# Optimization experiments

Hardware: AMD Instinct MI355X
Metric: run time of the kernel (lower is better)

## Reference

```python
import jax, jax.numpy as jnp
import numpy as np

D, E, H, K = 1024, 8, 1024, 2          # d_model, num_experts, hidden_size, top_k
NUM_LAYERS, LB_W, Z_W = 16, 0.01, 0.001
B, S = 2, 2048


def setup_inputs() -> dict:
    key = jax.random.key(0)
    ks = jax.random.split(key, 8)
    s = lambda d: 1.0 / np.sqrt(d)
    return {
        "x": jax.random.normal(ks[0], (B, S, D), jnp.float32),
        "w_router": jax.random.normal(ks[1], (D, E), jnp.float32) * s(D),
        "w1": jax.random.normal(ks[2], (E, D, H), jnp.float32) * s(D),
        "w3": jax.random.normal(ks[3], (E, D, H), jnp.float32) * s(D),
        "w2": jax.random.normal(ks[4], (E, H, D), jnp.float32) * s(H),
        "sw1": jax.random.normal(ks[5], (D, H), jnp.float32) * s(D),
        "sw3": jax.random.normal(ks[6], (D, H), jnp.float32) * s(D),
        "sw2": jax.random.normal(ks[7], (H, D), jnp.float32) * s(H),
    }


def reference(x, w_router, w1, w3, w2, sw1, sw3, sw2):
    b, s_len, _ = x.shape
    xt = x.reshape(-1, D)                       # (N, D) flattened tokens
    n_tok = xt.shape[0]

    # ---- router: softmax over experts, then top-k ----
    logits = xt @ w_router                      # (N, E)
    probs = jax.nn.softmax(logits, axis=-1)
    weights, indices = jax.lax.top_k(probs, K)  # (N, K)

    # combine weights scattered back to dense (N, E) form
    onehot = jax.nn.one_hot(indices, E, dtype=x.dtype)    # (N, K, E)
    cw = jnp.einsum("nk,nke->ne", weights, onehot)       # (N, E)
    counts = jnp.sum(onehot, axis=(0, 1))                 # (E,) tokens per expert

    # ---- expert SwiGLU MLPs (dense dispatch, weighted combine) ----
    g = jnp.einsum("nd,edh->neh", xt, w1)                 # (N, E, H)
    u = jnp.einsum("nd,edh->neh", xt, w3)
    h = jax.nn.silu(g) * u
    eout = jnp.einsum("neh,ehd->ned", h, w2)              # (N, E, D)
    out = jnp.einsum("ne,ned->nd", cw, eout)              # (N, D)

    # ---- shared expert, weighted-sum combine with top_k ----
    shared = (jax.nn.silu(xt @ sw1) * (xt @ sw3)) @ sw2   # (N, D)
    out = (out * K + shared) / (K + 1)

    # ---- aux losses (training mode) ----
    logits32 = logits.astype(jnp.float32)
    scale = E * LB_W / (NUM_LAYERS * n_tok * K)
    lb_loss = scale * jnp.dot(counts.astype(jnp.float32),
                              jax.nn.softmax(logits32, axis=-1).sum(axis=0))
    z_loss = jnp.mean(jnp.square(jax.nn.logsumexp(logits32, axis=-1))) * Z_W

    return out.reshape(b, s_len, D), lb_loss, z_loss
```

## Files before the change

kernel.cpp:

```cpp
#include <hip/hip_runtime.h>

#define NTOK 4096
#define NEXP 8
#define MAXTILES 104

typedef __attribute__((ext_vector_type(8))) short short8;
typedef __attribute__((ext_vector_type(4))) float f32x4;
typedef __attribute__((ext_vector_type(4))) unsigned int uint4v;
typedef __attribute__((ext_vector_type(2))) unsigned int uint2v;

__device__ __forceinline__ unsigned short f2bf(float f) {
  union { float f; unsigned u; } v; v.f = f;
  unsigned u = v.u;
  return (unsigned short)((u + 0x7FFFu + ((u >> 16) & 1u)) >> 16);
}

__device__ __forceinline__ void gll16(const void* g, void* l) {
  __builtin_amdgcn_global_load_lds((const __attribute__((address_space(1))) void*)g,
                                   (__attribute__((address_space(3))) void*)l, 16, 0, 0);
}

__global__ __launch_bounds__(256) void prep_k(
    const float* __restrict__ w1, const float* __restrict__ w3, const float* __restrict__ w2,
    const float* __restrict__ sw1, const float* __restrict__ sw3, const float* __restrict__ sw2,
    unsigned short* __restrict__ dst,
    const float* __restrict__ x, const float* __restrict__ wr, unsigned short* __restrict__ xb,
    int* __restrict__ rec, float* __restrict__ wts, float* __restrict__ probs,
    float* __restrict__ lsebuf) {
  __shared__ unsigned short tile[64][65];
  int b = blockIdx.x;
  if (b < 6912) {
    int z = b >> 8, rem = b & 255;
    int r0 = (rem >> 4) * 64, c0 = (rem & 15) * 64;
    const float* S;
    if (z < 8) S = w1 + (size_t)z * 1048576;
    else if (z < 16) S = w3 + (size_t)(z - 8) * 1048576;
    else if (z < 24) S = w2 + (size_t)(z - 16) * 1048576;
    else S = (z == 24) ? sw1 : (z == 25) ? sw3 : sw2;
    unsigned short* Dp = dst + (size_t)z * 1048576;
    int t = threadIdx.x;
    int r = t >> 2, cb = (t & 3) * 16;
    const float* sp = S + (size_t)(r0 + r) * 1024 + c0 + cb;
    f32x4 v0 = ((const f32x4*)sp)[0], v1 = ((const f32x4*)sp)[1];
    f32x4 v2 = ((const f32x4*)sp)[2], v3 = ((const f32x4*)sp)[3];
#pragma unroll
    for (int j = 0; j < 4; ++j) {
      tile[r][cb + j] = f2bf(v0[j]);
      tile[r][cb + 4 + j] = f2bf(v1[j]);
      tile[r][cb + 8 + j] = f2bf(v2[j]);
      tile[r][cb + 12 + j] = f2bf(v3[j]);
    }
    __syncthreads();
    unsigned short* dp = Dp + (size_t)(c0 + r) * 1024 + r0 + cb;
    uint4v o0, o1;
#pragma unroll
    for (int j = 0; j < 4; ++j) {
      o0[j] = (unsigned)tile[cb + 2 * j][r] | ((unsigned)tile[cb + 2 * j + 1][r] << 16);
      o1[j] = (unsigned)tile[cb + 8 + 2 * j][r] | ((unsigned)tile[cb + 9 + 2 * j][r] << 16);
    }
    ((uint4v*)dp)[0] = o0;
    ((uint4v*)dp)[1] = o1;
  } else {
    int t = threadIdx.x, lane = t & 63, wv = t >> 6;
    int tok = (b - 6912) * 4 + wv;
    const f32x4* x4 = (const f32x4*)(x + (size_t)tok * 1024);
    f32x4 xv[4];
#pragma unroll
    for (int j = 0; j < 4; ++j) xv[j] = x4[j * 64 + lane];

    unsigned short* xo = xb + (size_t)tok * 1024;
#pragma unroll
    for (int j = 0; j < 4; ++j) {
      uint2v o;
      o[0] = (unsigned)f2bf(xv[j][0]) | ((unsigned)f2bf(xv[j][1]) << 16);
      o[1] = (unsigned)f2bf(xv[j][2]) | ((unsigned)f2bf(xv[j][3]) << 16);
      *(uint2v*)(xo + j * 256 + lane * 4) = o;
    }

    float acc[NEXP];
#pragma unroll
    for (int e = 0; e < NEXP; ++e) acc[e] = 0.f;
#pragma unroll
    for (int j = 0; j < 4; ++j) {
      int base = j * 256 + lane * 4;
#pragma unroll
      for (int c = 0; c < 4; ++c) {
        float xf = xv[j][c];
        const f32x4* wp = (const f32x4*)(wr + (size_t)(base + c) * NEXP);
        f32x4 q0 = wp[0], q1 = wp[1];
#pragma unroll
        for (int e = 0; e < 4; ++e) { acc[e] += xf * q0[e]; acc[4 + e] += xf * q1[e]; }
      }
    }
#pragma unroll
    for (int off = 32; off > 0; off >>= 1) {
#pragma unroll
      for (int e = 0; e < NEXP; ++e) acc[e] += __shfl_xor(acc[e], off);
    }

    float mx = acc[0];
#pragma unroll
    for (int e = 1; e < NEXP; ++e) mx = fmaxf(mx, acc[e]);
    float s = 0.f;
#pragma unroll
    for (int e = 0; e < NEXP; ++e) s += __expf(acc[e] - mx);
    float inv = 1.f / s;

    if (lane < NEXP) probs[(size_t)tok * NEXP + lane] = __expf(acc[lane] - mx) * inv;
    if (lane == 0) {
      int i0 = 0; float v0 = acc[0];
#pragma unroll
      for (int e = 1; e < NEXP; ++e) if (acc[e] > v0) { v0 = acc[e]; i0 = e; }
      int i1 = -1; float v1 = -3.4e38f;
#pragma unroll
      for (int e = 0; e < NEXP; ++e) if (e != i0 && acc[e] > v1) { v1 = acc[e]; i1 = e; }
      rec[tok] = i0 | (i1 << 8);
      wts[2 * tok] = __expf(v0 - mx) * inv;
      wts[2 * tok + 1] = __expf(v1 - mx) * inv;
      lsebuf[tok] = mx + __logf(s);
    }
  }
}

__global__ __launch_bounds__(1024) void build_k(
    const int* __restrict__ rec, const float* __restrict__ wts, const float* __restrict__ probs,
    const float* __restrict__ lsebuf,
    int* __restrict__ tlist, float* __restrict__ wlist,
    int* __restrict__ counts, int* __restrict__ ebase, int* __restrict__ tiles,
    float* __restrict__ lossout) {
  __shared__ int lcnt[NEXP];
  __shared__ float sprob[NEXP];
  __shared__ float sz;
  int t = threadIdx.x, lane = t & 63;
  if (t < NEXP) { lcnt[t] = 0; sprob[t] = 0.f; }
  if (t == 0) sz = 0.f;
  __syncthreads();

  float pacc[NEXP];
#pragma unroll
  for (int e = 0; e < NEXP; ++e) pacc[e] = 0.f;
  float zacc = 0.f;

#pragma unroll
  for (int it = 0; it < 4; ++it) {
    int tok = t + it * 1024;
    int r = rec[tok];
    int i0 = r & 255, i1 = (r >> 8) & 255;
    int p0 = atomicAdd(&lcnt[i0], 1);
    tlist[i0 * NTOK + p0] = tok;
    wlist[i0 * NTOK + p0] = wts[2 * tok];
    int p1 = atomicAdd(&lcnt[i1], 1);
    tlist[i1 * NTOK + p1] = tok | (1 << 16);
    wlist[i1 * NTOK + p1] = wts[2 * tok + 1];
    f32x4 a = ((const f32x4*)(probs + (size_t)tok * NEXP))[0];
    f32x4 c = ((const f32x4*)(probs + (size_t)tok * NEXP))[1];
#pragma unroll
    for (int j = 0; j < 4; ++j) { pacc[j] += a[j]; pacc[4 + j] += c[j]; }
    float lv = lsebuf[tok];
    zacc += lv * lv;
  }
#pragma unroll
  for (int off = 32; off > 0; off >>= 1) {
#pragma unroll
    for (int e = 0; e < NEXP; ++e) pacc[e] += __shfl_xor(pacc[e], off);
    zacc += __shfl_xor(zacc, off);
  }
  if (lane == 0) {
#pragma unroll
    for (int e = 0; e < NEXP; ++e) atomicAdd(&sprob[e], pacc[e]);
    atomicAdd(&sz, zacc);
  }
  __syncthreads();

  if (t == 0) {
    int a = 0, tt = 0;
    float dot = 0.f;
    for (int e = 0; e < NEXP; ++e) {
      counts[e] = lcnt[e];
      ebase[e] = a;
      int nt = (lcnt[e] + 127) >> 7;
      for (int i = 0; i < nt; ++i) tiles[tt++] = (e << 16) | i;
      a += nt * 128;
      dot += (float)lcnt[e] * sprob[e];
    }
    ebase[NEXP] = a;
    for (int i = 0; i < 32; ++i) tiles[tt++] = (NEXP << 16) | i;
    while (tt < MAXTILES) tiles[tt++] = -1;
    lossout[0] = 6.103515625e-7f * dot;
    lossout[1] = sz * (0.001f / 4096.f);
  }
}

__global__ __launch_bounds__(256, 3) void gemm1_k(
    const unsigned short* __restrict__ xb,
    const unsigned short* __restrict__ w1T, const unsigned short* __restrict__ w3T,
    const unsigned short* __restrict__ sw1T, const unsigned short* __restrict__ sw3T,
    unsigned short* __restrict__ hout,
    const int* __restrict__ tlist, const int* __restrict__ counts,
    const int* __restrict__ ebase, const int* __restrict__ tiles) {
  int td = tiles[blockIdx.y];
  if (td < 0) return;
  const int e = td >> 16;
  const int m0 = (td & 0xFFFF) << 7;
  const int n0 = blockIdx.x * 64;
  const bool sh = (e == NEXP);
  const int n_e = sh ? NTOK : counts[e];
  const int hb = ebase[e];
  const unsigned short* B1p = sh ? sw1T : w1T + (size_t)e * 1048576;
  const unsigned short* B3p = sh ? sw3T : w3T + (size_t)e * 1048576;
  const int* listp = tlist + e * NTOK;

  __shared__ unsigned short As[128 * 64], Bs1[64 * 64], Bs3[64 * 64];
  const int tid = threadIdx.x, lane = tid & 63, wv = tid >> 6;
  const int wrw = wv >> 1, wc = wv & 1, l16 = lane & 15, lq = lane >> 4;

  const unsigned short* ga[4];
#pragma unroll
  for (int i = 0; i < 4; ++i) {
    int c = tid + i * 256;
    int r = c >> 3, ks = (c & 7) ^ (r & 7);
    int ar = m0 + r;
    int rowA = sh ? ar : (ar < n_e ? (listp[ar] & 0xFFFF) : 0);
    ga[i] = xb + (size_t)rowA * 1024 + ks * 8;
  }
  const unsigned short* gb[2];
  const unsigned short* gc[2];
#pragma unroll
  for (int i = 0; i < 2; ++i) {
    int c = tid + i * 256;
    int r = c >> 3, ks = (c & 7) ^ (r & 7);
    gb[i] = B1p + (size_t)(n0 + r) * 1024 + ks * 8;
    gc[i] = B3p + (size_t)(n0 + r) * 1024 + ks * 8;
  }
  unsigned short* lA[4];
#pragma unroll
  for (int i = 0; i < 4; ++i) lA[i] = As + i * 2048 + wv * 512;
  unsigned short* lB[2] = {Bs1 + wv * 512, Bs1 + 2048 + wv * 512};
  unsigned short* lC[2] = {Bs3 + wv * 512, Bs3 + 2048 + wv * 512};

  f32x4 accg[4][2], accu[4][2];
#pragma unroll
  for (int mi = 0; mi < 4; ++mi)
#pragma unroll
    for (int ni = 0; ni < 2; ++ni)
#pragma unroll
      for (int r = 0; r < 4; ++r) { accg[mi][ni][r] = 0.f; accu[mi][ni][r] = 0.f; }

  for (int k0 = 0; k0 < 1024; k0 += 64) {
#pragma unroll
    for (int i = 0; i < 4; ++i) { gll16(ga[i], lA[i]); ga[i] += 64; }
#pragma unroll
    for (int i = 0; i < 2; ++i) { gll16(gb[i], lB[i]); gb[i] += 64; gll16(gc[i], lC[i]); gc[i] += 64; }
    __syncthreads();
#pragma unroll
    for (int kh = 0; kh < 2; ++kh) {
      short8 af[4], b1f[2], b3f[2];
#pragma unroll
      for (int mi = 0; mi < 4; ++mi) {
        int R = wrw * 64 + mi * 16 + l16;
        int s = (kh * 4 + lq) ^ (R & 7);
        af[mi] = *(const short8*)&As[R * 64 + s * 8];
      }
#pragma unroll
      for (int ni = 0; ni < 2; ++ni) {
        int R = wc * 32 + ni * 16 + l16;
        int s = (kh * 4 + lq) ^ (R & 7);
        b1f[ni] = *(const short8*)&Bs1[R * 64 + s * 8];
        b3f[ni] = *(const short8*)&Bs3[R * 64 + s * 8];
      }
#pragma unroll
      for (int mi = 0; mi < 4; ++mi)
#pragma unroll
        for (int ni = 0; ni < 2; ++ni) {
          accg[mi][ni] = __builtin_amdgcn_mfma_f32_16x16x32_bf16(af[mi], b1f[ni], accg[mi][ni], 0, 0, 0);
          accu[mi][ni] = __builtin_amdgcn_mfma_f32_16x16x32_bf16(af[mi], b3f[ni], accu[mi][ni], 0, 0, 0);
        }
    }
    __syncthreads();
  }

#pragma unroll
  for (int mi = 0; mi < 4; ++mi)
#pragma unroll
    for (int ni = 0; ni < 2; ++ni) {
      int col = n0 + wc * 32 + ni * 16 + l16;
#pragma unroll
      for (int r = 0; r < 4; ++r) {
        int row = m0 + wrw * 64 + mi * 16 + lq * 4 + r;
        float g = accg[mi][ni][r], u = accu[mi][ni][r];
        float h = g / (1.f + __expf(-g)) * u;
        hout[(size_t)(hb + row) * 1024 + col] = (row < n_e) ? f2bf(h) : (unsigned short)0;
      }
    }
}

__global__ __launch_bounds__(256, 3) void gemm2_k(
    const unsigned short* __restrict__ hbuf,
    const unsigned short* __restrict__ w2T, const unsigned short* __restrict__ sw2T,
    float* __restrict__ yout,
    const int* __restrict__ tlist, const float* __restrict__ wlist,
    const int* __restrict__ counts, const int* __restrict__ ebase, const int* __restrict__ tiles) {
  int td = tiles[blockIdx.y];
  if (td < 0) return;
  const int e = td >> 16;
  const int m0 = (td & 0xFFFF) << 7;
  const int n0 = blockIdx.x * 128;
  const bool sh = (e == NEXP);
  const int n_e = sh ? NTOK : counts[e];
  const int hb = ebase[e];
  const unsigned short* Bp = sh ? sw2T : w2T + (size_t)e * 1048576;
  const int* listp = tlist + e * NTOK;

  __shared__ unsigned short As[128 * 64], Bs[128 * 64];
  const int tid = threadIdx.x, lane = tid & 63, wv = tid >> 6;
  const int wrw = wv >> 1, wc = wv & 1, l16 = lane & 15, lq = lane >> 4;

  const unsigned short* ga[4];
  const unsigned short* gb[4];
#pragma unroll
  for (int i = 0; i < 4; ++i) {
    int c = tid + i * 256;
    int r = c >> 3, ks = (c & 7) ^ (r & 7);
    ga[i] = hbuf + (size_t)(hb + m0 + r) * 1024 + ks * 8;
    gb[i] = Bp + (size_t)(n0 + r) * 1024 + ks * 8;
  }
  unsigned short* lA[4];
  unsigned short* lB[4];
#pragma unroll
  for (int i = 0; i < 4; ++i) {
    lA[i] = As + i * 2048 + wv * 512;
    lB[i] = Bs + i * 2048 + wv * 512;
  }

  f32x4 acc[4][4];
#pragma unroll
  for (int mi = 0; mi < 4; ++mi)
#pragma unroll
    for (int ni = 0; ni < 4; ++ni)
#pragma unroll
      for (int r = 0; r < 4; ++r) acc[mi][ni][r] = 0.f;

  for (int k0 = 0; k0 < 1024; k0 += 64) {
#pragma unroll
    for (int i = 0; i < 4; ++i) {
      gll16(ga[i], lA[i]); ga[i] += 64;
      gll16(gb[i], lB[i]); gb[i] += 64;
    }
    __syncthreads();
#pragma unroll
    for (int kh = 0; kh < 2; ++kh) {
      short8 af[4], bf[4];
#pragma unroll
      for (int mi = 0; mi < 4; ++mi) {
        int R = wrw * 64 + mi * 16 + l16;
        int s = (kh * 4 + lq) ^ (R & 7);
        af[mi] = *(const short8*)&As[R * 64 + s * 8];
      }
#pragma unroll
      for (int ni = 0; ni < 4; ++ni) {
        int R = wc * 64 + ni * 16 + l16;
        int s = (kh * 4 + lq) ^ (R & 7);
        bf[ni] = *(const short8*)&Bs[R * 64 + s * 8];
      }
#pragma unroll
      for (int mi = 0; mi < 4; ++mi)
#pragma unroll
        for (int ni = 0; ni < 4; ++ni)
          acc[mi][ni] = __builtin_amdgcn_mfma_f32_16x16x32_bf16(af[mi], bf[ni], acc[mi][ni], 0, 0, 0);
    }
    __syncthreads();
  }

#pragma unroll
  for (int mi = 0; mi < 4; ++mi)
#pragma unroll
    for (int r = 0; r < 4; ++r) {
      int row = m0 + wrw * 64 + mi * 16 + lq * 4 + r;
      if (sh) {
        float* yp = yout + ((size_t)2 * NTOK + row) * 1024 + n0 + wc * 64 + l16;
#pragma unroll
        for (int ni = 0; ni < 4; ++ni) yp[ni * 16] = acc[mi][ni][r] * (1.f / 3.f);
      } else if (row < n_e) {
        int ent = listp[row];
        float wt = wlist[e * NTOK + row] * (2.f / 3.f);
        int tok = ent & 0xFFFF, ks = ent >> 16;
        float* yp = yout + ((size_t)ks * NTOK + tok) * 1024 + n0 + wc * 64 + l16;
#pragma unroll
        for (int ni = 0; ni < 4; ++ni) yp[ni * 16] = wt * acc[mi][ni][r];
      }
    }
}

__global__ __launch_bounds__(256) void combine_k(const float* __restrict__ y,
                                                 float* __restrict__ out) {
  size_t i = (size_t)blockIdx.x * 256 + threadIdx.x;
  const f32x4* y0 = (const f32x4*)y + i;
  const f32x4* y1 = y0 + (NTOK * 1024 / 4);
  const f32x4* y2 = y1 + (NTOK * 1024 / 4);
  ((f32x4*)out)[i] = *y0 + *y1 + *y2;
}

extern "C" void kernel_launch(void* const* d_in, const int* in_sizes, int n_in,
                              void* d_out, int out_size, void* d_ws, size_t ws_size,
                              hipStream_t stream) {
  const float* x   = (const float*)d_in[0];
  const float* wrt = (const float*)d_in[1];
  const float* w1  = (const float*)d_in[2];
  const float* w3  = (const float*)d_in[3];
  const float* w2  = (const float*)d_in[4];
  const float* sw1 = (const float*)d_in[5];
  const float* sw3 = (const float*)d_in[6];
  const float* sw2 = (const float*)d_in[7];
  float* out = (float*)d_out;

  char* p = (char*)d_ws;
  auto alloc = [&](size_t b) { char* r = p; p += (b + 255) & ~(size_t)255; return r; };
  unsigned short* xb   = (unsigned short*)alloc((size_t)NTOK * 1024 * 2);
  unsigned short* w1T  = (unsigned short*)alloc((size_t)27 * 1048576 * 2);
  unsigned short* w3T  = w1T + (size_t)8 * 1048576;
  unsigned short* w2T  = w3T + (size_t)8 * 1048576;
  unsigned short* sw1T = w2T + (size_t)8 * 1048576;
  unsigned short* sw3T = sw1T + 1048576;
  unsigned short* sw2T = sw3T + 1048576;
  unsigned short* hbuf = (unsigned short*)alloc((size_t)13312 * 1024 * 2);
  float* ybuf   = (float*)alloc((size_t)3 * NTOK * 1024 * 4);
  int* tlist    = (int*)alloc((size_t)NEXP * NTOK * 4);
  float* wlist  = (float*)alloc((size_t)NEXP * NTOK * 4);
  int* rec      = (int*)alloc((size_t)NTOK * 4);
  float* wts    = (float*)alloc((size_t)NTOK * 2 * 4);
  float* probs  = (float*)alloc((size_t)NTOK * NEXP * 4);
  float* lsebuf = (float*)alloc((size_t)NTOK * 4);
  int* tiles    = (int*)alloc(MAXTILES * 4);
  int* ebase    = (int*)alloc(256);
  int* counts   = (int*)alloc(256);

  prep_k<<<7936, 256, 0, stream>>>(w1, w3, w2, sw1, sw3, sw2, w1T,
                                   x, wrt, xb, rec, wts, probs, lsebuf);
  build_k<<<1, 1024, 0, stream>>>(rec, wts, probs, lsebuf, tlist, wlist,
                                  counts, ebase, tiles, out + (size_t)NTOK * 1024);
  gemm1_k<<<dim3(16, MAXTILES), 256, 0, stream>>>(xb, w1T, w3T, sw1T, sw3T, hbuf, tlist, counts, ebase, tiles);
  gemm2_k<<<dim3(8, MAXTILES), 256, 0, stream>>>(hbuf, w2T, sw2T, ybuf, tlist, wlist, counts, ebase, tiles);
  combine_k<<<NTOK * 1024 / 4 / 256, 256, 0, stream>>>(ybuf, out);
}
```

Before: 315.8 us.

## Overlap w2 transpose with gemm1, shrink gemm2 tile, write shared output directly

```diff
diff --git a/kernel.cpp b/kernel.cpp
--- a/kernel.cpp
+++ b/kernel.cpp
@@ -20,49 +20,54 @@
                                    (__attribute__((address_space(3))) void*)l, 16, 0, 0);
 }
 
+__device__ __forceinline__ void transpose_tile(const float* __restrict__ S,
+                                               unsigned short* __restrict__ Dp,
+                                               int r0, int c0, int t,
+                                               unsigned short (*tile)[65]) {
+  int r = t >> 2, cb = (t & 3) * 16;
+  const float* sp = S + (size_t)(r0 + r) * 1024 + c0 + cb;
+  f32x4 v0 = ((const f32x4*)sp)[0], v1 = ((const f32x4*)sp)[1];
+  f32x4 v2 = ((const f32x4*)sp)[2], v3 = ((const f32x4*)sp)[3];
+#pragma unroll
+  for (int j = 0; j < 4; ++j) {
+    tile[r][cb + j] = f2bf(v0[j]);
+    tile[r][cb + 4 + j] = f2bf(v1[j]);
+    tile[r][cb + 8 + j] = f2bf(v2[j]);
+    tile[r][cb + 12 + j] = f2bf(v3[j]);
+  }
+  __syncthreads();
+  unsigned short* dp = Dp + (size_t)(c0 + r) * 1024 + r0 + cb;
+  uint4v o0, o1;
+#pragma unroll
+  for (int j = 0; j < 4; ++j) {
+    o0[j] = (unsigned)tile[cb + 2 * j][r] | ((unsigned)tile[cb + 2 * j + 1][r] << 16);
+    o1[j] = (unsigned)tile[cb + 8 + 2 * j][r] | ((unsigned)tile[cb + 9 + 2 * j][r] << 16);
+  }
+  ((uint4v*)dp)[0] = o0;
+  ((uint4v*)dp)[1] = o1;
+}
+
 __global__ __launch_bounds__(256) void prep_k(
-    const float* __restrict__ w1, const float* __restrict__ w3, const float* __restrict__ w2,
-    const float* __restrict__ sw1, const float* __restrict__ sw3, const float* __restrict__ sw2,
-    unsigned short* __restrict__ dst,
+    const float* __restrict__ w1, const float* __restrict__ w3,
+    const float* __restrict__ sw1, const float* __restrict__ sw3,
+    unsigned short* __restrict__ dst ,
     const float* __restrict__ x, const float* __restrict__ wr, unsigned short* __restrict__ xb,
     int* __restrict__ rec, float* __restrict__ wts, float* __restrict__ probs,
     float* __restrict__ lsebuf) {
   __shared__ unsigned short tile[64][65];
   int b = blockIdx.x;
-  if (b < 6912) {
+  if (b < 4608) {
     int z = b >> 8, rem = b & 255;
-    int r0 = (rem >> 4) * 64, c0 = (rem & 15) * 64;
     const float* S;
-    if (z < 8) S = w1 + (size_t)z * 1048576;
-    else if (z < 16) S = w3 + (size_t)(z - 8) * 1048576;
-    else if (z < 24) S = w2 + (size_t)(z - 16) * 1048576;
-    else S = (z == 24) ? sw1 : (z == 25) ? sw3 : sw2;
-    unsigned short* Dp = dst + (size_t)z * 1048576;
-    int t = threadIdx.x;
-    int r = t >> 2, cb = (t & 3) * 16;
-    const float* sp = S + (size_t)(r0 + r) * 1024 + c0 + cb;
-    f32x4 v0 = ((const f32x4*)sp)[0], v1 = ((const f32x4*)sp)[1];
-    f32x4 v2 = ((const f32x4*)sp)[2], v3 = ((const f32x4*)sp)[3];
-#pragma unroll
-    for (int j = 0; j < 4; ++j) {
-      tile[r][cb + j] = f2bf(v0[j]);
-      tile[r][cb + 4 + j] = f2bf(v1[j]);
-      tile[r][cb + 8 + j] = f2bf(v2[j]);
-      tile[r][cb + 12 + j] = f2bf(v3[j]);
-    }
-    __syncthreads();
-    unsigned short* dp = Dp + (size_t)(c0 + r) * 1024 + r0 + cb;
-    uint4v o0, o1;
-#pragma unroll
-    for (int j = 0; j < 4; ++j) {
-      o0[j] = (unsigned)tile[cb + 2 * j][r] | ((unsigned)tile[cb + 2 * j + 1][r] << 16);
-      o1[j] = (unsigned)tile[cb + 8 + 2 * j][r] | ((unsigned)tile[cb + 9 + 2 * j][r] << 16);
-    }
-    ((uint4v*)dp)[0] = o0;
-    ((uint4v*)dp)[1] = o1;
+    unsigned short* Dp;
+    if (z < 8) { S = w1 + (size_t)z * 1048576; Dp = dst + (size_t)z * 1048576; }
+    else if (z < 16) { S = w3 + (size_t)(z - 8) * 1048576; Dp = dst + (size_t)z * 1048576; }
+    else if (z == 16) { S = sw1; Dp = dst + (size_t)24 * 1048576; }
+    else { S = sw3; Dp = dst + (size_t)25 * 1048576; }
+    transpose_tile(S, Dp, (rem >> 4) * 64, (rem & 15) * 64, threadIdx.x, tile);
   } else {
     int t = threadIdx.x, lane = t & 63, wv = t >> 6;
-    int tok = (b - 6912) * 4 + wv;
+    int tok = (b - 4608) * 4 + wv;
     const f32x4* x4 = (const f32x4*)(x + (size_t)tok * 1024);
     f32x4 xv[4];
 #pragma unroll
@@ -197,7 +202,23 @@
     const unsigned short* __restrict__ sw1T, const unsigned short* __restrict__ sw3T,
     unsigned short* __restrict__ hout,
     const int* __restrict__ tlist, const int* __restrict__ counts,
-    const int* __restrict__ ebase, const int* __restrict__ tiles) {
+    const int* __restrict__ ebase, const int* __restrict__ tiles,
+    const float* __restrict__ w2, const float* __restrict__ sw2,
+    unsigned short* __restrict__ wTbase ) {
+  __shared__ unsigned short As[128 * 64], Bs1[64 * 64], Bs3[64 * 64];
+  const int tid = threadIdx.x;
+
+  if (blockIdx.y >= MAXTILES) {
+    int tb = (blockIdx.y - MAXTILES) * 16 + blockIdx.x;
+    int z = tb >> 8, rem = tb & 255;
+    const float* S = (z < 8) ? w2 + (size_t)z * 1048576 : sw2;
+    unsigned short* Dp = (z < 8) ? wTbase + (size_t)(16 + z) * 1048576
+                                 : wTbase + (size_t)26 * 1048576;
+    transpose_tile(S, Dp, (rem >> 4) * 64, (rem & 15) * 64, tid,
+                   (unsigned short (*)[65])As);
+    return;
+  }
+
   int td = tiles[blockIdx.y];
   if (td < 0) return;
   const int e = td >> 16;
@@ -210,8 +231,7 @@
   const unsigned short* B3p = sh ? sw3T : w3T + (size_t)e * 1048576;
   const int* listp = tlist + e * NTOK;
 
-  __shared__ unsigned short As[128 * 64], Bs1[64 * 64], Bs3[64 * 64];
-  const int tid = threadIdx.x, lane = tid & 63, wv = tid >> 6;
+  const int lane = tid & 63, wv = tid >> 6;
   const int wrw = wv >> 1, wc = wv & 1, l16 = lane & 15, lq = lane >> 4;
 
   const unsigned short* ga[4];
@@ -294,62 +314,63 @@
     }
 }
 
-__global__ __launch_bounds__(256, 3) void gemm2_k(
+__global__ __launch_bounds__(256, 4) void gemm2_k(
     const unsigned short* __restrict__ hbuf,
     const unsigned short* __restrict__ w2T, const unsigned short* __restrict__ sw2T,
-    float* __restrict__ yout,
+    float* __restrict__ ybuf, float* __restrict__ out,
     const int* __restrict__ tlist, const float* __restrict__ wlist,
     const int* __restrict__ counts, const int* __restrict__ ebase, const int* __restrict__ tiles) {
   int td = tiles[blockIdx.y];
   if (td < 0) return;
   const int e = td >> 16;
   const int m0 = (td & 0xFFFF) << 7;
-  const int n0 = blockIdx.x * 128;
+  const int n0 = blockIdx.x * 64;
   const bool sh = (e == NEXP);
   const int n_e = sh ? NTOK : counts[e];
   const int hb = ebase[e];
   const unsigned short* Bp = sh ? sw2T : w2T + (size_t)e * 1048576;
   const int* listp = tlist + e * NTOK;
 
-  __shared__ unsigned short As[128 * 64], Bs[128 * 64];
+  __shared__ unsigned short As[128 * 64], Bs[64 * 64];
   const int tid = threadIdx.x, lane = tid & 63, wv = tid >> 6;
   const int wrw = wv >> 1, wc = wv & 1, l16 = lane & 15, lq = lane >> 4;
 
   const unsigned short* ga[4];
-  const unsigned short* gb[4];
 #pragma unroll
   for (int i = 0; i < 4; ++i) {
     int c = tid + i * 256;
     int r = c >> 3, ks = (c & 7) ^ (r & 7);
     ga[i] = hbuf + (size_t)(hb + m0 + r) * 1024 + ks * 8;
+  }
+  const unsigned short* gb[2];
+#pragma unroll
+  for (int i = 0; i < 2; ++i) {
+    int c = tid + i * 256;
+    int r = c >> 3, ks = (c & 7) ^ (r & 7);
     gb[i] = Bp + (size_t)(n0 + r) * 1024 + ks * 8;
   }
   unsigned short* lA[4];
-  unsigned short* lB[4];
-#pragma unroll
-  for (int i = 0; i < 4; ++i) {
-    lA[i] = As + i * 2048 + wv * 512;
-    lB[i] = Bs + i * 2048 + wv * 512;
-  }
-
-  f32x4 acc[4][4];
+#pragma unroll
+  for (int i = 0; i < 4; ++i) lA[i] = As + i * 2048 + wv * 512;
+  unsigned short* lB[2] = {Bs + wv * 512, Bs + 2048 + wv * 512};
+
+  f32x4 acc[4][2];
 #pragma unroll
   for (int mi = 0; mi < 4; ++mi)
 #pragma unroll
-    for (int ni = 0; ni < 4; ++ni)
+    for (int ni = 0; ni < 2; ++ni)
 #pragma unroll
       for (int r = 0; r < 4; ++r) acc[mi][ni][r] = 0.f;
 
   for (int k0 = 0; k0 < 1024; k0 += 64) {
 #pragma unroll
-    for (int i = 0; i < 4; ++i) {
-      gll16(ga[i], lA[i]); ga[i] += 64;
-      gll16(gb[i], lB[i]); gb[i] += 64;
-    }
+    for (int i = 0; i < 4; ++i) { gll16(ga[i], lA[i]); ga[i] += 64; }
+#pragma unroll
+    for (int i = 0; i < 2; ++i) { gll16(gb[i], lB[i]); gb[i] += 64; }
     __syncthreads();
 #pragma unroll
     for (int kh = 0; kh < 2; ++kh) {
-      short8 af[4], bf[4];
+      short8 af[4], bf[2];
 #pragma unroll
       for (int mi = 0; mi < 4; ++mi) {
         int R = wrw * 64 + mi * 16 + l16;
@@ -357,15 +378,15 @@
         af[mi] = *(const short8*)&As[R * 64 + s * 8];
       }
 #pragma unroll
-      for (int ni = 0; ni < 4; ++ni) {
-        int R = wc * 64 + ni * 16 + l16;
+      for (int ni = 0; ni < 2; ++ni) {
+        int R = wc * 32 + ni * 16 + l16;
         int s = (kh * 4 + lq) ^ (R & 7);
         bf[ni] = *(const short8*)&Bs[R * 64 + s * 8];
       }
 #pragma unroll
       for (int mi = 0; mi < 4; ++mi)
 #pragma unroll
-        for (int ni = 0; ni < 4; ++ni)
+        for (int ni = 0; ni < 2; ++ni)
           acc[mi][ni] = __builtin_amdgcn_mfma_f32_16x16x32_bf16(af[mi], bf[ni], acc[mi][ni], 0, 0, 0);
     }
     __syncthreads();
@@ -376,17 +397,18 @@
 #pragma unroll
     for (int r = 0; r < 4; ++r) {
       int row = m0 + wrw * 64 + mi * 16 + lq * 4 + r;
+      int col = n0 + wc * 32 + l16;
       if (sh) {
-        float* yp = yout + ((size_t)2 * NTOK + row) * 1024 + n0 + wc * 64 + l16;
-#pragma unroll
-        for (int ni = 0; ni < 4; ++ni) yp[ni * 16] = acc[mi][ni][r] * (1.f / 3.f);
+        float* yp = out + (size_t)row * 1024 + col;
+#pragma unroll
+        for (int ni = 0; ni < 2; ++ni) yp[ni * 16] = acc[mi][ni][r] * (1.f / 3.f);
       } else if (row < n_e) {
         int ent = listp[row];
         float wt = wlist[e * NTOK + row] * (2.f / 3.f);
         int tok = ent & 0xFFFF, ks = ent >> 16;
-        float* yp = yout + ((size_t)ks * NTOK + tok) * 1024 + n0 + wc * 64 + l16;
-#pragma unroll
-        for (int ni = 0; ni < 4; ++ni) yp[ni * 16] = wt * acc[mi][ni][r];
+        float* yp = ybuf + ((size_t)ks * NTOK + tok) * 1024 + col;
+#pragma unroll
+        for (int ni = 0; ni < 2; ++ni) yp[ni * 16] = wt * acc[mi][ni][r];
       }
     }
 }
@@ -396,8 +418,8 @@
   size_t i = (size_t)blockIdx.x * 256 + threadIdx.x;
   const f32x4* y0 = (const f32x4*)y + i;
   const f32x4* y1 = y0 + (NTOK * 1024 / 4);
-  const f32x4* y2 = y1 + (NTOK * 1024 / 4);
-  ((f32x4*)out)[i] = *y0 + *y1 + *y2;
+  f32x4 o = ((f32x4*)out)[i];
+  ((f32x4*)out)[i] = o + *y0 + *y1;
 }
 
 extern "C" void kernel_launch(void* const* d_in, const int* in_sizes, int n_in,
@@ -423,7 +445,7 @@
   unsigned short* sw3T = sw1T + 1048576;
   unsigned short* sw2T = sw3T + 1048576;
   unsigned short* hbuf = (unsigned short*)alloc((size_t)13312 * 1024 * 2);
-  float* ybuf   = (float*)alloc((size_t)3 * NTOK * 1024 * 4);
+  float* ybuf   = (float*)alloc((size_t)2 * NTOK * 1024 * 4);
   int* tlist    = (int*)alloc((size_t)NEXP * NTOK * 4);
   float* wlist  = (float*)alloc((size_t)NEXP * NTOK * 4);
   int* rec      = (int*)alloc((size_t)NTOK * 4);
@@ -434,11 +456,13 @@
   int* ebase    = (int*)alloc(256);
   int* counts   = (int*)alloc(256);
 
-  prep_k<<<7936, 256, 0, stream>>>(w1, w3, w2, sw1, sw3, sw2, w1T,
+  prep_k<<<5632, 256, 0, stream>>>(w1, w3, sw1, sw3, w1T,
                                    x, wrt, xb, rec, wts, probs, lsebuf);
   build_k<<<1, 1024, 0, stream>>>(rec, wts, probs, lsebuf, tlist, wlist,
                                   counts, ebase, tiles, out + (size_t)NTOK * 1024);
-  gemm1_k<<<dim3(16, MAXTILES), 256, 0, stream>>>(xb, w1T, w3T, sw1T, sw3T, hbuf, tlist, counts, ebase, tiles);
-  gemm2_k<<<dim3(8, MAXTILES), 256, 0, stream>>>(hbuf, w2T, sw2T, ybuf, tlist, wlist, counts, ebase, tiles);
+  gemm1_k<<<dim3(16, MAXTILES + 144), 256, 0, stream>>>(
+      xb, w1T, w3T, sw1T, sw3T, hbuf, tlist, counts, ebase, tiles, w2, sw2, w1T);
+  gemm2_k<<<dim3(16, MAXTILES), 256, 0, stream>>>(hbuf, w2T, sw2T, ybuf, out,
+                                                  tlist, wlist, counts, ebase, tiles);
   combine_k<<<NTOK * 1024 / 4 / 256, 256, 0, stream>>>(ybuf, out);
 }
```

After: 303.8 us. -3.8%, faster.
